# Kernel tuning notes

Measured on AMD Instinct MI355X. Metric: run time of the kernel, lower is better.

The kernel has to match this reference:

```python
import jax, jax.numpy as jnp
import numpy as np
from jax import lax

BETA = 0.5
IPOT_ITERS = 20


def cosine_cost(x, y):
    # x: [bs, n, D], y: [bs, m, D] -> 1 - cos_sim, [bs, n, m]
    x = x / (jnp.linalg.norm(x, axis=2, keepdims=True) + 1e-12)
    y = y / (jnp.linalg.norm(y, axis=2, keepdims=True) + 1e-12)
    return 1.0 - jnp.einsum('bnd,bmd->bnm', x, y)


def ipot_T(C, miu, nu, beta=BETA, iters=IPOT_ITERS):
    bs, n, m = C.shape
    A = jnp.exp(-C / beta)                    # [bs, n, m]
    sigma0 = jnp.ones((bs, m, 1), C.dtype) / m
    T0 = jnp.ones((bs, n, m), C.dtype)

    def step(carry, _):
        T, sigma = carry
        T = A * T
        delta = miu[:, :, None] / (T @ sigma + 1e-6)            # [bs, n, 1]
        sigma = nu[:, :, None] / (jnp.swapaxes(T, 1, 2) @ delta + 1e-6)  # [bs, m, 1]
        T = delta * T * jnp.swapaxes(sigma, 1, 2)
        return (T, sigma), None

    (T, _), _ = lax.scan(step, (T0, sigma0), None, length=iters)
    return lax.stop_gradient(T)  # original code detaches T


def ipot_distance(C):
    bs, n, m = C.shape
    miu = jnp.ones((bs, n), C.dtype) / n
    nu = jnp.ones((bs, m), C.dtype) / m
    T = ipot_T(C, miu, nu)
    return -jnp.sum(T * C, axis=(1, 2))  # note: original (un-exponentiated) C


def setup_inputs() -> dict:
    key = jax.random.key(0)
    k1, k2, k3, k4 = jax.random.split(key, 4)
    bs, n_sp, n_tm, D = 128, 196, 32, 768
    return {
        'spatial1': jax.random.normal(k1, (bs, n_sp, D), dtype=jnp.float32),
        'spatial2': jax.random.normal(k2, (bs, n_sp, D), dtype=jnp.float32),
        'temporal1': jax.random.normal(k3, (bs, n_tm, D), dtype=jnp.float32),
        'temporal2': jax.random.normal(k4, (bs, n_tm, D), dtype=jnp.float32),
    }


def reference(spatial1, spatial2, temporal1, temporal2):
    C_sp = cosine_cost(spatial1, spatial2)
    C_tm = cosine_cost(temporal1, temporal2)
    spatial_loss = ipot_distance(C_sp)
    temporal_loss = ipot_distance(C_tm)
    return spatial_loss.mean() + temporal_loss.mean()
```

## Files before the change

### kernel.cpp

```cpp
#include <hip/hip_runtime.h>
#include <hip/hip_bf16.h>
#include <cstdint>

typedef float f32x4 __attribute__((ext_vector_type(4)));
typedef __bf16 bf16x8 __attribute__((ext_vector_type(8)));

#define BS 128
#define NSP 196
#define NTM 32
#define DDIM 768

__device__ inline ushort4 f4_to_bf4(float4 v)
{
    ushort4 u;
    u.x = __builtin_bit_cast(unsigned short, (__bf16)v.x);
    u.y = __builtin_bit_cast(unsigned short, (__bf16)v.y);
    u.z = __builtin_bit_cast(unsigned short, (__bf16)v.z);
    u.w = __builtin_bit_cast(unsigned short, (__bf16)v.w);
    return u;
}

__device__ inline bf16x8 f4x2_to_bf8(float4 lo, float4 hi)
{
    bf16x8 r;
    r[0] = (__bf16)lo.x; r[1] = (__bf16)lo.y; r[2] = (__bf16)lo.z; r[3] = (__bf16)lo.w;
    r[4] = (__bf16)hi.x; r[5] = (__bf16)hi.y; r[6] = (__bf16)hi.z; r[7] = (__bf16)hi.w;
    return r;
}

__device__ inline float sumsq4(float4 a)
{
    return fmaf(a.x, a.x, fmaf(a.y, a.y, fmaf(a.z, a.z, a.w * a.w)));
}

__device__ inline float row16_sum(float x)
{
    int t;
    t = __builtin_amdgcn_update_dpp(0, __builtin_bit_cast(int, x), 0x121, 0xf, 0xf, true);
    x += __builtin_bit_cast(float, t);
    t = __builtin_amdgcn_update_dpp(0, __builtin_bit_cast(int, x), 0x122, 0xf, 0xf, true);
    x += __builtin_bit_cast(float, t);
    t = __builtin_amdgcn_update_dpp(0, __builtin_bit_cast(int, x), 0x124, 0xf, 0xf, true);
    x += __builtin_bit_cast(float, t);
    t = __builtin_amdgcn_update_dpp(0, __builtin_bit_cast(int, x), 0x128, 0xf, 0xf, true);
    x += __builtin_bit_cast(float, t);
    return x;
}

__global__ __launch_bounds__(256)
void tm_norm_kernel(const float* __restrict__ tm1, const float* __restrict__ tm2,
                    float* __restrict__ inx_tm, float* __restrict__ iny_tm)
{
    int B = blockIdx.x;
    const float* src; float* inv;
    if (B < 1024) { src = tm1; inv = inx_tm; }
    else          { B -= 1024; src = tm2; inv = iny_tm; }
    const int row  = B * 4 + (threadIdx.x >> 6);
    const int lane = threadIdx.x & 63;
    const float4* p = reinterpret_cast<const float4*>(src + (size_t)row * DDIM);
    float ss = 0.f;
#pragma unroll
    for (int c = 0; c < 3; ++c) ss += sumsq4(p[lane + 64 * c]);
#pragma unroll
    for (int off = 32; off; off >>= 1) ss += __shfl_xor(ss, off, 64);
    if (lane == 0) inv[row] = 1.0f / (sqrtf(ss) + 1e-12f);
}

#define GA_LDS 18432
__global__ __launch_bounds__(448)
void cost_gemm_spf(const float* __restrict__ X, const float* __restrict__ Y,
                   __bf16* __restrict__ Aout)
{
    __shared__ __bf16 lds[2 * GA_LDS];
    float* ldsF = reinterpret_cast<float*>(lds);

    const int flat  = blockIdx.x;
    const int xcd   = flat & 7;
    const int s     = flat >> 3;
    const int b     = xcd * 16 + (s >> 2);
    const int ctile = s & 3;
    const int n0    = (ctile < 3) ? ctile * 64 : 132;

    const int tid  = threadIdx.x;
    const int w    = tid >> 6, lane = tid & 63;
    const int q    = lane >> 4, l16 = lane & 15;
    const int srow = tid >> 3;
    const int sslt = tid & 7;

    const float* Yb = Y + (size_t)b * NSP * DDIM;

    float4 aL[4], aH[4], bL, bH, b2L, b2H;
    float ssA[4] = {0.f, 0.f, 0.f, 0.f};
    float ssB = 0.f, ssB2 = 0.f;

    auto LOADS = [&](int k0) {
#pragma unroll
        for (int p = 0; p < 4; ++p) {
            int gr = b * NSP + srow + 56 * p;
            gr = min(gr, BS * NSP - 1);
            const float* sp = X + (size_t)gr * DDIM + k0 + sslt * 8;
            aL[p] = *reinterpret_cast<const float4*>(sp);
            aH[p] = *reinterpret_cast<const float4*>(sp + 4);
        }
        {
            const float* sp = Yb + (size_t)(n0 + srow) * DDIM + k0 + sslt * 8;
            bL = *reinterpret_cast<const float4*>(sp);
            bH = *reinterpret_cast<const float4*>(sp + 4);
        }
        if (tid < 64) {
            const float* sp = Yb + (size_t)(n0 + 56 + srow) * DDIM + k0 + sslt * 8;
            b2L = *reinterpret_cast<const float4*>(sp);
            b2H = *reinterpret_cast<const float4*>(sp + 4);
        }
    };
    auto WRITES = [&](int buf) {
#pragma unroll
        for (int p = 0; p < 4; ++p) {
            int r = srow + 56 * p;
            ssA[p] += sumsq4(aL[p]) + sumsq4(aH[p]);
            *reinterpret_cast<bf16x8*>(&lds[buf * GA_LDS + r * 64 + ((sslt ^ (r & 7)) << 3)]) =
                f4x2_to_bf8(aL[p], aH[p]);
        }
        {
            int r = srow;
            ssB += sumsq4(bL) + sumsq4(bH);
            *reinterpret_cast<bf16x8*>(&lds[buf * GA_LDS + 14336 + r * 64 + ((sslt ^ (r & 7)) << 3)]) =
                f4x2_to_bf8(bL, bH);
        }
        if (tid < 64) {
            int r = 56 + srow;
            ssB2 += sumsq4(b2L) + sumsq4(b2H);
            *reinterpret_cast<bf16x8*>(&lds[buf * GA_LDS + 14336 + r * 64 + ((sslt ^ (r & 7)) << 3)]) =
                f4x2_to_bf8(b2L, b2H);
        }
    };

    f32x4 acc[2][4];
#pragma unroll
    for (int i = 0; i < 2; ++i)
#pragma unroll
        for (int j = 0; j < 4; ++j) acc[i][j] = f32x4{0.f, 0.f, 0.f, 0.f};

    LOADS(0);
    int buf = 0;
    for (int kt = 0; kt < 12; ++kt) {
        WRITES(buf);
        if (kt < 11) LOADS((kt + 1) * 64);
        __syncthreads();
#pragma unroll
        for (int ks = 0; ks < 2; ++ks) {
            bf16x8 af[2], bf[4];
#pragma unroll
            for (int rt = 0; rt < 2; ++rt) {
                int r = w * 32 + rt * 16 + l16;
                af[rt] = *reinterpret_cast<const bf16x8*>(
                    &lds[buf * GA_LDS + r * 64 + (((ks * 4 + q) ^ (r & 7)) << 3)]);
            }
#pragma unroll
            for (int ct = 0; ct < 4; ++ct) {
                int r = ct * 16 + l16;
                bf[ct] = *reinterpret_cast<const bf16x8*>(
                    &lds[buf * GA_LDS + 14336 + r * 64 + (((ks * 4 + q) ^ (r & 7)) << 3)]);
            }
#pragma unroll
            for (int ct = 0; ct < 4; ++ct)
#pragma unroll
                for (int rt = 0; rt < 2; ++rt)
                    acc[rt][ct] = __builtin_amdgcn_mfma_f32_16x16x32_bf16(af[rt], bf[ct], acc[rt][ct], 0, 0, 0);
        }
        __syncthreads();
        buf ^= 1;
    }

#pragma unroll
    for (int p = 0; p < 4; ++p) ldsF[(srow + 56 * p) * 8 + sslt] = ssA[p];
    ldsF[1792 + srow * 8 + sslt] = ssB;
    if (tid < 64) ldsF[1792 + (56 + srow) * 8 + sslt] = ssB2;
    __syncthreads();

    float ivy[4];
#pragma unroll
    for (int ct = 0; ct < 4; ++ct) {
        int jr = ct * 16 + l16;
        f32x4 s0 = *reinterpret_cast<const f32x4*>(&ldsF[1792 + jr * 8]);
        f32x4 s1 = *reinterpret_cast<const f32x4*>(&ldsF[1792 + jr * 8 + 4]);
        float ss = (s0.x + s0.y) + (s0.z + s0.w) + (s1.x + s1.y) + (s1.z + s1.w);
        ivy[ct] = 1.0f / (sqrtf(ss) + 1e-12f);
    }
#pragma unroll
    for (int rt = 0; rt < 2; ++rt)
#pragma unroll
        for (int rr = 0; rr < 4; ++rr) {
            int i = w * 32 + rt * 16 + q * 4 + rr;
            if (i < NSP) {
                f32x4 s0 = *reinterpret_cast<const f32x4*>(&ldsF[i * 8]);
                f32x4 s1 = *reinterpret_cast<const f32x4*>(&ldsF[i * 8 + 4]);
                float ss = (s0.x + s0.y) + (s0.z + s0.w) + (s1.x + s1.y) + (s1.z + s1.w);
                float ivx = 1.0f / (sqrtf(ss) + 1e-12f);
#pragma unroll
                for (int ct = 0; ct < 4; ++ct) {
                    float cs = acc[rt][ct][rr] * ivx * ivy[ct];
                    Aout[(size_t)b * 65536 + (size_t)i * 256 + (n0 + ct * 16 + l16)] =
                        (__bf16)__expf(2.0f * cs - 2.0f);
                }
            }
        }
}

template<int WROWS, int NWAVES, int BN, int NPTS>
__global__ __launch_bounds__(NWAVES * 64)
void cost_gemm(const float* __restrict__ X, const float* __restrict__ Y,
               const float* __restrict__ invx, const float* __restrict__ invy,
               float* __restrict__ Aout)
{
    constexpr int MT = WROWS * NWAVES;
    constexpr int CT = BN / 16;
    constexpr int RT = WROWS / 16;
    constexpr int KP = 40;
    constexpr int NTH = NWAVES * 64;
    __shared__ __bf16 As[MT][KP];
    __shared__ __bf16 Bs[BN][KP];

    const int b    = blockIdx.y;
    const int row0 = blockIdx.x * MT;
    const int tid  = threadIdx.x;
    const int w    = tid >> 6, lane = tid & 63;
    const int q    = lane >> 4, l16 = lane & 15;
    const float* Xb = X + (size_t)b * NPTS * DDIM;
    const float* Yb = Y + (size_t)b * NPTS * DDIM;

    f32x4 acc[RT][CT];
#pragma unroll
    for (int i = 0; i < RT; ++i)
#pragma unroll
        for (int j = 0; j < CT; ++j) acc[i][j] = f32x4{0.f, 0.f, 0.f, 0.f};

    for (int k0 = 0; k0 < DDIM; k0 += 32) {
        __syncthreads();
        for (int idx = tid * 4; idx < MT * 32; idx += NTH * 4) {
            int r = idx >> 5, kk = idx & 31;
            int gr = row0 + r;
            float4 v = {0.f, 0.f, 0.f, 0.f};
            if (gr < NPTS) v = *reinterpret_cast<const float4*>(Xb + (size_t)gr * DDIM + k0 + kk);
            *reinterpret_cast<ushort4*>(&As[r][kk]) = f4_to_bf4(v);
        }
        for (int idx = tid * 4; idx < BN * 32; idx += NTH * 4) {
            int r = idx >> 5, kk = idx & 31;
            float4 v = {0.f, 0.f, 0.f, 0.f};
            if (r < NPTS) v = *reinterpret_cast<const float4*>(Yb + (size_t)r * DDIM + k0 + kk);
            *reinterpret_cast<ushort4*>(&Bs[r][kk]) = f4_to_bf4(v);
        }
        __syncthreads();

        bf16x8 af[RT];
#pragma unroll
        for (int rt = 0; rt < RT; ++rt)
            af[rt] = *reinterpret_cast<const bf16x8*>(&As[w * WROWS + rt * 16 + l16][q * 8]);
#pragma unroll
        for (int ct = 0; ct < CT; ++ct) {
            bf16x8 bfr = *reinterpret_cast<const bf16x8*>(&Bs[ct * 16 + l16][q * 8]);
#pragma unroll
            for (int rt = 0; rt < RT; ++rt)
                acc[rt][ct] = __builtin_amdgcn_mfma_f32_16x16x32_bf16(af[rt], bfr, acc[rt][ct], 0, 0, 0);
        }
    }

#pragma unroll
    for (int rt = 0; rt < RT; ++rt)
#pragma unroll
        for (int ct = 0; ct < CT; ++ct)
#pragma unroll
            for (int rr = 0; rr < 4; ++rr) {
                int i = row0 + w * WROWS + rt * 16 + q * 4 + rr;
                int j = ct * 16 + l16;
                if (i < NPTS && j < NPTS) {
                    float g  = acc[rt][ct][rr];
                    float cs = g * invx[b * NPTS + i] * invy[b * NPTS + j];
                    Aout[(size_t)b * NPTS * NPTS + (size_t)i * NPTS + j] = expf(-2.0f * (1.0f - cs));
                }
            }
}

__global__ __launch_bounds__(512, 1)
void ipot_dpp(const __bf16* __restrict__ Asp, const float* __restrict__ Atm,
              float* __restrict__ out)
{
    __shared__ __bf16 Alds[224 * 256];
    __shared__ float  cpart[32 * 260];
    __shared__ float  svec[2][272];
    __shared__ float  wsum[8];

    const int B = blockIdx.x;
    if (B >= 128) {
        if (threadIdx.x >= 64) return;
        const int b = B - 128;
        const float* Ab = Atm + (size_t)b * NTM * NTM;
        const int lane = threadIdx.x;
        const int rh = lane >> 5, cj = lane & 31;
        constexpr float MIU = 1.f / NTM;
        float A[16], P[16];
#pragma unroll
        for (int k = 0; k < 16; ++k) {
            A[k] = Ab[(rh + 2 * k) * NTM + cj];
            P[k] = 1.f;
        }
        float sv = MIU;
        for (int it = 0; it < 20; ++it) {
#pragma unroll
            for (int k = 0; k < 16; ++k) {
                P[k] *= A[k];
                float acc = row16_sum(P[k] * sv);
                acc += __shfl_xor(acc, 16);
                P[k] *= MIU * __builtin_amdgcn_rcpf(acc + 1e-6f);
            }
            float cssum = 0.f;
#pragma unroll
            for (int k = 0; k < 16; ++k) cssum += P[k];
            cssum += __shfl_xor(cssum, 32);
            float sg = MIU * __builtin_amdgcn_rcpf(cssum + 1e-6f);
#pragma unroll
            for (int k = 0; k < 16; ++k) P[k] *= sg;
            sv = sg;
        }
        float acc = 0.f;
#pragma unroll
        for (int k = 0; k < 16; ++k)
            acc = fmaf(P[k], -0.5f * __logf(A[k]), acc);
        acc = row16_sum(acc);
        acc += __shfl_xor(acc, 16);
        acc += __shfl_xor(acc, 32);
        if (lane == 0) atomicAdd(out, -acc * (1.f / BS));
        return;
    }

    const int b = (B & 7) * 16 + (B >> 3);
    const __bf16* Ab = Asp + (size_t)b * 65536;
    const int tid = threadIdx.x;
    const int w = tid >> 6, lane = tid & 63;
    const int rq = lane >> 4, cl = lane & 15;
    const int g = w * 4 + rq;
    const int colbase = cl * 8;
    constexpr float MIU = 1.f / NSP;

    for (int idx = tid; idx < NSP * 32; idx += 512) {
        int r = idx >> 5, c = idx & 31;
        bf16x8 v;
#pragma unroll
        for (int i = 0; i < 8; ++i) v[i] = (__bf16)0.f;
        if (c < 25) {
            v = *reinterpret_cast<const bf16x8*>(&Ab[(size_t)r * 256 + c * 8]);
            if (c == 24) { v[4] = (__bf16)0.f; v[5] = (__bf16)0.f; v[6] = (__bf16)0.f; v[7] = (__bf16)0.f; }
        }
        *reinterpret_cast<bf16x8*>(&Alds[r * 256 + c * 8]) = v;
    }
    {
        ushort4 z = {0, 0, 0, 0};
        for (int idx = tid; idx < 28 * 64; idx += 512) {
            int r = 196 + (idx >> 6), c4 = (idx & 63) << 2;
            *reinterpret_cast<ushort4*>(&Alds[r * 256 + c4]) = z;
        }
    }
    __syncthreads();

    float P[7][16];
#pragma unroll
    for (int k = 0; k < 7; ++k)
#pragma unroll
        for (int e = 0; e < 16; ++e) P[k][e] = 1.f;

    float sr[16];
#pragma unroll
    for (int e = 0; e < 16; ++e) {
        int j = (e < 8) ? (colbase + e) : (colbase + 128 + (e - 8));
        sr[e] = (j < NSP) ? MIU : 0.f;
    }

    for (int it = 0; it < 20; ++it) {
        float cs[16];
#pragma unroll
        for (int e = 0; e < 16; ++e) cs[e] = 0.f;

#pragma unroll
        for (int k = 0; k < 7; ++k) {
            const __bf16* ap = &Alds[(g + 32 * k) * 256 + colbase];
            bf16x8 a0 = *reinterpret_cast<const bf16x8*>(ap);
            bf16x8 a1 = *reinterpret_cast<const bf16x8*>(ap + 128);
            float r0 = 0.f, r1 = 0.f;
#pragma unroll
            for (int e = 0; e < 8; ++e) {
                P[k][e] *= (float)a0[e];
                r0 = fmaf(P[k][e], sr[e], r0);
            }
#pragma unroll
            for (int e = 0; e < 8; ++e) {
                P[k][8 + e] *= (float)a1[e];
                r1 = fmaf(P[k][8 + e], sr[8 + e], r1);
            }
            float racc = row16_sum(r0 + r1);
            float delta = MIU * __builtin_amdgcn_rcpf(racc + 1e-6f);
#pragma unroll
            for (int e = 0; e < 16; ++e) {
                P[k][e] *= delta;
                cs[e] += P[k][e];
            }
        }
        {
            float* cp = &cpart[g * 260 + colbase];
            *reinterpret_cast<f32x4*>(cp)     = f32x4{cs[0], cs[1], cs[2], cs[3]};
            *reinterpret_cast<f32x4*>(cp + 4) = f32x4{cs[4], cs[5], cs[6], cs[7]};
            float* cp2 = cp + 128;
            *reinterpret_cast<f32x4*>(cp2)     = f32x4{cs[8], cs[9], cs[10], cs[11]};
            *reinterpret_cast<f32x4*>(cp2 + 4) = f32x4{cs[12], cs[13], cs[14], cs[15]};
        }
        __syncthreads();
        if (tid < 256) {
            float s0 = 0.f, s1 = 0.f, s2 = 0.f, s3 = 0.f;
#pragma unroll
            for (int gg = 0; gg < 32; gg += 4) {
                s0 += cpart[(gg + 0) * 260 + tid];
                s1 += cpart[(gg + 1) * 260 + tid];
                s2 += cpart[(gg + 2) * 260 + tid];
                s3 += cpart[(gg + 3) * 260 + tid];
            }
            float sum = (s0 + s1) + (s2 + s3);
            svec[it & 1][tid] = (tid < NSP) ? (MIU * __builtin_amdgcn_rcpf(sum + 1e-6f)) : 0.f;
        }
        __syncthreads();
        {
            const float* sv = svec[it & 1];
            f32x4 t0 = *reinterpret_cast<const f32x4*>(&sv[colbase]);
            f32x4 t1 = *reinterpret_cast<const f32x4*>(&sv[colbase + 4]);
            f32x4 t2 = *reinterpret_cast<const f32x4*>(&sv[colbase + 128]);
            f32x4 t3 = *reinterpret_cast<const f32x4*>(&sv[colbase + 132]);
            sr[0] = t0.x; sr[1] = t0.y; sr[2] = t0.z; sr[3] = t0.w;
            sr[4] = t1.x; sr[5] = t1.y; sr[6] = t1.z; sr[7] = t1.w;
            sr[8] = t2.x; sr[9] = t2.y; sr[10] = t2.z; sr[11] = t2.w;
            sr[12] = t3.x; sr[13] = t3.y; sr[14] = t3.z; sr[15] = t3.w;
        }
#pragma unroll
        for (int k = 0; k < 7; ++k)
#pragma unroll
            for (int e = 0; e < 16; ++e) P[k][e] *= sr[e];
    }

    float acc = 0.f;
#pragma unroll
    for (int k = 0; k < 7; ++k) {
        const __bf16* ap = &Alds[(g + 32 * k) * 256 + colbase];
        bf16x8 a0 = *reinterpret_cast<const bf16x8*>(ap);
        bf16x8 a1 = *reinterpret_cast<const bf16x8*>(ap + 128);
#pragma unroll
        for (int e = 0; e < 8; ++e) {
            acc = fmaf(P[k][e],     -0.5f * __logf(fmaxf((float)a0[e], 1e-30f)), acc);
            acc = fmaf(P[k][8 + e], -0.5f * __logf(fmaxf((float)a1[e], 1e-30f)), acc);
        }
    }
    acc = row16_sum(acc);
    acc += __shfl_xor(acc, 16);
    acc += __shfl_xor(acc, 32);
    if (lane == 0) wsum[w] = acc;
    __syncthreads();
    if (tid == 0) {
        float t = 0.f;
#pragma unroll
        for (int i = 0; i < 8; ++i) t += wsum[i];
        atomicAdd(out, -t * (1.f / BS));
    }
}

extern "C" void kernel_launch(void* const* d_in, const int* in_sizes, int n_in,
                              void* d_out, int out_size, void* d_ws, size_t ws_size,
                              hipStream_t stream)
{
    const float* sp1 = (const float*)d_in[0];
    const float* sp2 = (const float*)d_in[1];
    const float* tm1 = (const float*)d_in[2];
    const float* tm2 = (const float*)d_in[3];
    float* out = (float*)d_out;
    float* ws  = (float*)d_ws;

    float* inx_tm = ws;
    float* iny_tm = inx_tm + BS * NTM;
    float* A_tm   = iny_tm + BS * NTM;
    __bf16* A_sp  = (__bf16*)(ws + 139264);

    tm_norm_kernel<<<dim3(2048), 256, 0, stream>>>(tm1, tm2, inx_tm, iny_tm);

    cost_gemm_spf<<<dim3(512), 448, 0, stream>>>(sp1, sp2, A_sp);

    cost_gemm<16, 2, 32, NTM><<<dim3(1, BS), 128, 0, stream>>>(tm1, tm2, inx_tm, iny_tm, A_tm);

    (void)hipMemsetAsync(d_out, 0, sizeof(float), stream);

    ipot_dpp<<<dim3(256), 512, 0, stream>>>(A_sp, A_tm, out);
}
```

Baseline: 159.9 us.

## Retile spatial cost GEMM into 128-row blocks with deeper A prefetch

Replaces the 448-thread spatial cosine-cost GEMM with a 256-thread kernel. Each block covers a 128-row by 64-column tile, giving 1024 blocks, and the kernel asks for 3 blocks per SIMD via launch bounds. The X operand is prefetched two k-steps ahead in double register buffers, and the trailing per-iteration barrier is dropped because the double-buffered LDS already separates reads from writes. The aim is more parallelism and better latency hiding in the global-load-bound GEMM. The cost is idle padded rows in the second row tile (only 68 of its 128 rows are valid) and more register pressure.

Result: slower. 298.4 us (+86.5%).

```diff
diff --git a/kernel.cpp b/kernel.cpp
--- a/kernel.cpp
+++ b/kernel.cpp
@@ -18,14 +18,6 @@
     u.z = __builtin_bit_cast(unsigned short, (__bf16)v.z);
     u.w = __builtin_bit_cast(unsigned short, (__bf16)v.w);
     return u;
-}
-
-__device__ inline bf16x8 f4x2_to_bf8(float4 lo, float4 hi)
-{
-    bf16x8 r;
-    r[0] = (__bf16)lo.x; r[1] = (__bf16)lo.y; r[2] = (__bf16)lo.z; r[3] = (__bf16)lo.w;
-    r[4] = (__bf16)hi.x; r[5] = (__bf16)hi.y; r[6] = (__bf16)hi.z; r[7] = (__bf16)hi.w;
-    return r;
 }
 
 __device__ inline float sumsq4(float4 a)
@@ -66,74 +58,70 @@
     if (lane == 0) inv[row] = 1.0f / (sqrtf(ss) + 1e-12f);
 }
 
-#define GA_LDS 18432
-__global__ __launch_bounds__(448)
-void cost_gemm_spf(const float* __restrict__ X, const float* __restrict__ Y,
-                   __bf16* __restrict__ Aout)
-{
-    __shared__ __bf16 lds[2 * GA_LDS];
+#define V2_LDSE 12288
+__global__ __launch_bounds__(256, 3)
+void cost_gemm_v2(const float* __restrict__ X, const float* __restrict__ Y,
+                  __bf16* __restrict__ Aout)
+{
+    __shared__ __bf16 lds[2 * V2_LDSE];
     float* ldsF = reinterpret_cast<float*>(lds);
 
-    const int flat  = blockIdx.x;
-    const int xcd   = flat & 7;
-    const int s     = flat >> 3;
-    const int b     = xcd * 16 + (s >> 2);
-    const int ctile = s & 3;
-    const int n0    = (ctile < 3) ? ctile * 64 : 132;
-
-    const int tid  = threadIdx.x;
-    const int w    = tid >> 6, lane = tid & 63;
-    const int q    = lane >> 4, l16 = lane & 15;
-    const int srow = tid >> 3;
-    const int sslt = tid & 7;
-
-    const float* Yb = Y + (size_t)b * NSP * DDIM;
-
-    float4 aL[4], aH[4], bL, bH, b2L, b2H;
-    float ssA[4] = {0.f, 0.f, 0.f, 0.f};
-    float ssB = 0.f, ssB2 = 0.f;
-
-    auto LOADS = [&](int k0) {
-#pragma unroll
-        for (int p = 0; p < 4; ++p) {
-            int gr = b * NSP + srow + 56 * p;
-            gr = min(gr, BS * NSP - 1);
-            const float* sp = X + (size_t)gr * DDIM + k0 + sslt * 8;
-            aL[p] = *reinterpret_cast<const float4*>(sp);
-            aH[p] = *reinterpret_cast<const float4*>(sp + 4);
-        }
-        {
-            const float* sp = Yb + (size_t)(n0 + srow) * DDIM + k0 + sslt * 8;
-            bL = *reinterpret_cast<const float4*>(sp);
-            bH = *reinterpret_cast<const float4*>(sp + 4);
-        }
-        if (tid < 64) {
-            const float* sp = Yb + (size_t)(n0 + 56 + srow) * DDIM + k0 + sslt * 8;
-            b2L = *reinterpret_cast<const float4*>(sp);
-            b2H = *reinterpret_cast<const float4*>(sp + 4);
-        }
+    const int flat = blockIdx.x;
+    const int xcd  = flat & 7;
+    const int s    = flat >> 3;
+    const int b    = xcd * 16 + (s >> 3);
+    const int rt_  = (s >> 2) & 1;
+    const int ct_  = s & 3;
+    const int r0   = rt_ * 128;
+    const int n0   = (ct_ < 3) ? ct_ * 64 : 132;
+
+    const int tid = threadIdx.x;
+    const int w = tid >> 6, lane = tid & 63;
+    const int q = lane >> 4, l16 = lane & 15;
+    const int rA  = tid >> 4;
+    const int kq  = tid & 15;
+    const int slt = kq >> 1;
+    const int hof = (kq & 1) * 4;
+
+    const float* Yb = Y + ((size_t)b * NSP + n0) * DDIM;
+
+    int arow[8];
+#pragma unroll
+    for (int j = 0; j < 8; ++j) {
+        int ri = r0 + rA + 16 * j;
+        arow[j] = b * NSP + min(ri, NSP - 1);
+    }
+
+    float4 aR[2][8], bR[4];
+    float ssA[8] = {0.f, 0.f, 0.f, 0.f, 0.f, 0.f, 0.f, 0.f};
+    float ssB[4] = {0.f, 0.f, 0.f, 0.f};
+
+    auto LOADSA = [&](int d, int k0) {
+#pragma unroll
+        for (int j = 0; j < 8; ++j)
+            aR[d][j] = *reinterpret_cast<const float4*>(X + (size_t)arow[j] * DDIM + k0 + kq * 4);
     };
-    auto WRITES = [&](int buf) {
-#pragma unroll
-        for (int p = 0; p < 4; ++p) {
-            int r = srow + 56 * p;
-            ssA[p] += sumsq4(aL[p]) + sumsq4(aH[p]);
-            *reinterpret_cast<bf16x8*>(&lds[buf * GA_LDS + r * 64 + ((sslt ^ (r & 7)) << 3)]) =
-                f4x2_to_bf8(aL[p], aH[p]);
-        }
-        {
-            int r = srow;
-            ssB += sumsq4(bL) + sumsq4(bH);
-            *reinterpret_cast<bf16x8*>(&lds[buf * GA_LDS + 14336 + r * 64 + ((sslt ^ (r & 7)) << 3)]) =
-                f4x2_to_bf8(bL, bH);
-        }
-        if (tid < 64) {
-            int r = 56 + srow;
-            ssB2 += sumsq4(b2L) + sumsq4(b2H);
-            *reinterpret_cast<bf16x8*>(&lds[buf * GA_LDS + 14336 + r * 64 + ((sslt ^ (r & 7)) << 3)]) =
-                f4x2_to_bf8(b2L, b2H);
-        }
+    auto LOADSB = [&](int k0) {
+#pragma unroll
+        for (int j = 0; j < 4; ++j)
+            bR[j] = *reinterpret_cast<const float4*>(Yb + (size_t)(rA + 16 * j) * DDIM + k0 + kq * 4);
     };
+    auto WRITES = [&](int d, int buf) {
+#pragma unroll
+        for (int j = 0; j < 8; ++j) {
+            int r = rA + 16 * j;
+            ssA[j] += sumsq4(aR[d][j]);
+            *reinterpret_cast<ushort4*>(&lds[buf * V2_LDSE + r * 64 + ((slt ^ (r & 7)) << 3) + hof]) =
+                f4_to_bf4(aR[d][j]);
+        }
+#pragma unroll
+        for (int j = 0; j < 4; ++j) {
+            int r = rA + 16 * j;
+            ssB[j] += sumsq4(bR[j]);
+            *reinterpret_cast<ushort4*>(&lds[buf * V2_LDSE + 8192 + r * 64 + ((slt ^ (r & 7)) << 3) + hof]) =
+                f4_to_bf4(bR[j]);
+        }
+    };
 
     f32x4 acc[2][4];
 #pragma unroll
@@ -141,66 +129,68 @@
 #pragma unroll
         for (int j = 0; j < 4; ++j) acc[i][j] = f32x4{0.f, 0.f, 0.f, 0.f};
 
-    LOADS(0);
+    LOADSB(0);
+    LOADSA(0, 0);
+    LOADSA(1, 64);
     int buf = 0;
     for (int kt = 0; kt < 12; ++kt) {
-        WRITES(buf);
-        if (kt < 11) LOADS((kt + 1) * 64);
+        WRITES(kt & 1, buf);
+        if (kt < 11) LOADSB((kt + 1) * 64);
+        if (kt < 10) LOADSA(kt & 1, (kt + 2) * 64);
         __syncthreads();
 #pragma unroll
         for (int ks = 0; ks < 2; ++ks) {
-            bf16x8 af[2], bf[4];
+            bf16x8 af[2], bfr[4];
 #pragma unroll
             for (int rt = 0; rt < 2; ++rt) {
                 int r = w * 32 + rt * 16 + l16;
                 af[rt] = *reinterpret_cast<const bf16x8*>(
-                    &lds[buf * GA_LDS + r * 64 + (((ks * 4 + q) ^ (r & 7)) << 3)]);
+                    &lds[buf * V2_LDSE + r * 64 + (((ks * 4 + q) ^ (r & 7)) << 3)]);
             }
 #pragma unroll
             for (int ct = 0; ct < 4; ++ct) {
                 int r = ct * 16 + l16;
-                bf[ct] = *reinterpret_cast<const bf16x8*>(
-                    &lds[buf * GA_LDS + 14336 + r * 64 + (((ks * 4 + q) ^ (r & 7)) << 3)]);
+                bfr[ct] = *reinterpret_cast<const bf16x8*>(
+                    &lds[buf * V2_LDSE + 8192 + r * 64 + (((ks * 4 + q) ^ (r & 7)) << 3)]);
             }
 #pragma unroll
             for (int ct = 0; ct < 4; ++ct)
 #pragma unroll
                 for (int rt = 0; rt < 2; ++rt)
-                    acc[rt][ct] = __builtin_amdgcn_mfma_f32_16x16x32_bf16(af[rt], bf[ct], acc[rt][ct], 0, 0, 0);
-        }
-        __syncthreads();
+                    acc[rt][ct] = __builtin_amdgcn_mfma_f32_16x16x32_bf16(af[rt], bfr[ct], acc[rt][ct], 0, 0, 0);
+        }
         buf ^= 1;
     }
-
-#pragma unroll
-    for (int p = 0; p < 4; ++p) ldsF[(srow + 56 * p) * 8 + sslt] = ssA[p];
-    ldsF[1792 + srow * 8 + sslt] = ssB;
-    if (tid < 64) ldsF[1792 + (56 + srow) * 8 + sslt] = ssB2;
+    __syncthreads();
+
+#pragma unroll
+    for (int j = 0; j < 8; ++j) ldsF[(rA + 16 * j) * 16 + kq] = ssA[j];
+#pragma unroll
+    for (int j = 0; j < 4; ++j) ldsF[2048 + (rA + 16 * j) * 16 + kq] = ssB[j];
     __syncthreads();
 
     float ivy[4];
 #pragma unroll
     for (int ct = 0; ct < 4; ++ct) {
         int jr = ct * 16 + l16;
-        f32x4 s0 = *reinterpret_cast<const f32x4*>(&ldsF[1792 + jr * 8]);
-        f32x4 s1 = *reinterpret_cast<const f32x4*>(&ldsF[1792 + jr * 8 + 4]);
-        float ss = (s0.x + s0.y) + (s0.z + s0.w) + (s1.x + s1.y) + (s1.z + s1.w);
-        ivy[ct] = 1.0f / (sqrtf(ss) + 1e-12f);
+        const f32x4* p = reinterpret_cast<const f32x4*>(&ldsF[2048 + jr * 16]);
+        f32x4 t = p[0] + p[1] + p[2] + p[3];
+        ivy[ct] = 1.0f / (sqrtf((t.x + t.y) + (t.z + t.w)) + 1e-12f);
     }
 #pragma unroll
     for (int rt = 0; rt < 2; ++rt)
 #pragma unroll
         for (int rr = 0; rr < 4; ++rr) {
             int i = w * 32 + rt * 16 + q * 4 + rr;
-            if (i < NSP) {
-                f32x4 s0 = *reinterpret_cast<const f32x4*>(&ldsF[i * 8]);
-                f32x4 s1 = *reinterpret_cast<const f32x4*>(&ldsF[i * 8 + 4]);
-                float ss = (s0.x + s0.y) + (s0.z + s0.w) + (s1.x + s1.y) + (s1.z + s1.w);
-                float ivx = 1.0f / (sqrtf(ss) + 1e-12f);
+            int gi = r0 + i;
+            if (gi < NSP) {
+                const f32x4* p = reinterpret_cast<const f32x4*>(&ldsF[i * 16]);
+                f32x4 t = p[0] + p[1] + p[2] + p[3];
+                float ivx = 1.0f / (sqrtf((t.x + t.y) + (t.z + t.w)) + 1e-12f);
 #pragma unroll
                 for (int ct = 0; ct < 4; ++ct) {
                     float cs = acc[rt][ct][rr] * ivx * ivy[ct];
-                    Aout[(size_t)b * 65536 + (size_t)i * 256 + (n0 + ct * 16 + l16)] =
+                    Aout[(size_t)b * 65536 + (size_t)gi * 256 + (n0 + ct * 16 + l16)] =
                         (__bf16)__expf(2.0f * cs - 2.0f);
                 }
             }
@@ -486,7 +476,7 @@
 
     tm_norm_kernel<<<dim3(2048), 256, 0, stream>>>(tm1, tm2, inx_tm, iny_tm);
 
-    cost_gemm_spf<<<dim3(512), 448, 0, stream>>>(sp1, sp2, A_sp);
+    cost_gemm_v2<<<dim3(1024), 256, 0, stream>>>(sp1, sp2, A_sp);
 
     cost_gemm<16, 2, 32, NTM><<<dim3(1, BS), 128, 0, stream>>>(tm1, tm2, inx_tm, iny_tm, A_tm);
 
```
